# Performance work log

Hardware: AMD Instinct MI355X
Metric: run time of the kernel (lower is better)

Reference implementation:

```python
import jax, jax.numpy as jnp
import numpy as np

B, NIN, H1, H2, NOUT, COND, FC = 64, 512, 1024, 1024, 512, 64, 1


def _made_masks():
    rng = np.random.RandomState(0)
    d_in = np.arange(1, NIN + 1)
    d1 = rng.randint(1, NIN, size=H1)
    d2 = rng.randint(1, NIN, size=H2)
    d_out = np.arange(1, NOUT + 1)
    m0 = (d1[:, None] >= d_in[None, :]).astype(np.float32)   # (H1, NIN)
    m1 = (d2[:, None] >= d1[None, :]).astype(np.float32)     # (H2, H1)
    m2 = (d_out[:, None] > d2[None, :]).astype(np.float32)   # (NOUT, H2)
    return m0, m1, m2


def setup_inputs() -> dict:
    key = jax.random.key(0)
    ks = jax.random.split(key, 20)
    m0, m1, m2 = _made_masks()

    def lin(k, o, i):  # fan-in scaled weight
        return jax.random.normal(k, (o, i), jnp.float32) / np.float32(np.sqrt(i))

    def vec(k, n):
        return jax.random.normal(k, (n,), jnp.float32) * 0.01

    return {
        "x": jax.random.normal(ks[0], (B, NIN), jnp.float32),
        "u": jax.random.normal(ks[1], (B, COND), jnp.float32),
        "mask0": jnp.asarray(m0), "mask1": jnp.asarray(m1), "mask2": jnp.asarray(m2),
        "W0": lin(ks[2], H1, NIN), "W1": lin(ks[3], H2, H1), "W2": lin(ks[4], NOUT, H2),
        "a0_w": lin(ks[5], FC * NIN, COND), "a0_b": vec(ks[6], FC * NIN),
        "b0_w": lin(ks[7], FC * H1, COND), "b0_b": vec(ks[8], FC * H1),
        "a1_w": lin(ks[9], FC * H1, COND), "a1_b": vec(ks[10], FC * H1),
        "b1_w": lin(ks[11], FC * H2, COND), "b1_b": vec(ks[12], FC * H2),
        "a2_w": lin(ks[13], FC * H2, COND), "a2_b": vec(ks[14], FC * H2),
        "b2_w": lin(ks[15], FC * NOUT, COND), "b2_b": vec(ks[16], FC * NOUT),
    }


def _cml(x, u, W, m, aw, ab, bw, bb):
    # ConditionedMaskedLinear.forward
    Bb = x.shape[0]
    o, i = W.shape
    f1 = (u @ aw.T + ab).reshape(Bb, FC, i)      # (B, F, in)
    f2 = (u @ bw.T + bb).reshape(Bb, o, FC)      # (B, out, F)
    cond_mask = jax.nn.sigmoid(jnp.einsum('bfi,bof->boi', f1, f2)) * (m * W)
    return jnp.einsum('boi,bi->bo', cond_mask, x)


def reference(x, u, mask0, mask1, mask2, W0, W1, W2,
              a0_w, a0_b, b0_w, b0_b,
              a1_w, a1_b, b1_w, b1_b,
              a2_w, a2_b, b2_w, b2_b):
    # ConditionalStrNN.forward applies ONLY the ConditionedMaskedLinear layers
    # (activations/norms in net_list are skipped by the isinstance check).
    h = _cml(x, u, W0, mask0, a0_w, a0_b, b0_w, b0_b)
    h = _cml(h, u, W1, mask1, a1_w, a1_b, b1_w, b1_b)
    h = _cml(h, u, W2, mask2, a2_w, a2_b, b2_w, b2_b)
    return h
```

## Files before the change

### kernel.cpp

```cpp
#include <hip/hip_runtime.h>

#define BB    64
#define NIN   512
#define H1D   1024
#define H2D   1024
#define NOUTD 512
#define CONDD 64
#define L2E   1.4426950408889634f

__global__ __launch_bounds__(256) void prep_kernel(
    const float* __restrict__ x,  const float* __restrict__ u,
    const float* __restrict__ a0w, const float* __restrict__ a0b,
    const float* __restrict__ b0w, const float* __restrict__ b0b,
    const float* __restrict__ a1w, const float* __restrict__ a1b,
    const float* __restrict__ b1w, const float* __restrict__ b1b,
    const float* __restrict__ a2w, const float* __restrict__ a2b,
    const float* __restrict__ b2w, const float* __restrict__ b2b,
    float* __restrict__ AX0, float* __restrict__ AX1, float* __restrict__ AX2,
    float* __restrict__ C0t, float* __restrict__ C1t, float* __restrict__ C2t)
{
    __shared__ float lds[64 * 65];
    const int tid = threadIdx.x;
    const int bid = blockIdx.x;

    if (bid < 320) {
        for (int e = tid; e < BB * CONDD; e += 256)
            lds[(e & 63) * 65 + (e >> 6)] = u[e];
        __syncthreads();

        const int b   = tid & 63;
        const int wid = __builtin_amdgcn_readfirstlane(tid >> 6);
        const int r0  = bid * 16 + wid * 4;

        const float* w; const float* bias; float* out; int stride; float scale; int lr0;
        if      (r0 <  512) { w = a0w; bias = a0b; out = AX0; stride = 2; scale = L2E; lr0 = r0;        }
        else if (r0 < 1536) { w = b0w; bias = b0b; out = C0t; stride = 1; scale = 1.f; lr0 = r0 -  512; }
        else if (r0 < 2560) { w = a1w; bias = a1b; out = AX1; stride = 2; scale = L2E; lr0 = r0 - 1536; }
        else if (r0 < 3584) { w = b1w; bias = b1b; out = C1t; stride = 1; scale = 1.f; lr0 = r0 - 2560; }
        else if (r0 < 4608) { w = a2w; bias = a2b; out = AX2; stride = 2; scale = L2E; lr0 = r0 - 3584; }
        else                { w = b2w; bias = b2b; out = C2t; stride = 1; scale = 1.f; lr0 = r0 - 4608; }

        const float* __restrict__ w0 = w + (lr0 + 0) * CONDD;
        const float* __restrict__ w1 = w + (lr0 + 1) * CONDD;
        const float* __restrict__ w2 = w + (lr0 + 2) * CONDD;
        const float* __restrict__ w3 = w + (lr0 + 3) * CONDD;
        float acc0 = bias[lr0 + 0], acc1 = bias[lr0 + 1];
        float acc2 = bias[lr0 + 2], acc3 = bias[lr0 + 3];
        #pragma unroll
        for (int k = 0; k < CONDD; ++k) {
            const float uv = lds[k * 65 + b];
            acc0 = fmaf(w0[k], uv, acc0);
            acc1 = fmaf(w1[k], uv, acc1);
            acc2 = fmaf(w2[k], uv, acc2);
            acc3 = fmaf(w3[k], uv, acc3);
        }
        out[((lr0 + 0) * 64 + b) * stride] = acc0 * scale;
        out[((lr0 + 1) * 64 + b) * stride] = acc1 * scale;
        out[((lr0 + 2) * 64 + b) * stride] = acc2 * scale;
        out[((lr0 + 3) * 64 + b) * stride] = acc3 * scale;
    } else {
        const int i0 = (bid - 320) * 64;
        for (int e = tid; e < 64 * 64; e += 256) {
            int r = e >> 6, c = e & 63;
            lds[c * 65 + r] = x[r * NIN + i0 + c];
        }
        __syncthreads();
        for (int e = tid; e < 64 * 64; e += 256) {
            int r = e >> 6, c = e & 63;
            AX0[((i0 + r) * 64 + c) * 2 + 1] = lds[r * 65 + c];
        }
    }
}

template<int I, int OT, bool FINAL>
__device__ __forceinline__ void gated_body(
    const float2* __restrict__ AX, const float* __restrict__ Ct,
    const float*  __restrict__ M,  const float* __restrict__ W,
    float* __restrict__ out)
{
    constexpr int ICW = I / 8;
    const int tid = threadIdx.x;
    const int b   = tid & 63;
    const int wid = __builtin_amdgcn_readfirstlane(tid >> 6);
    const int o0  = blockIdx.x * OT;
    const int ibase = wid * ICW;

    float cc[OT], acc[OT];
    const float* __restrict__ mrow[OT];
    const float* __restrict__ wrow[OT];
    #pragma unroll
    for (int oo = 0; oo < OT; ++oo) {
        cc[oo]   = Ct[(o0 + oo) * 64 + b];
        mrow[oo] = M + (size_t)(o0 + oo) * I + ibase;
        wrow[oo] = W + (size_t)(o0 + oo) * I + ibase;
        acc[oo]  = 0.f;
    }
    const float2* __restrict__ axp = AX + (size_t)ibase * 64 + b;

    #pragma unroll 8
    for (int ii = 0; ii < ICW; ++ii) {
        const float2 ax = axp[(size_t)ii * 64];
        #pragma unroll
        for (int oo = 0; oo < OT; ++oo) {
            const float mw = mrow[oo][ii] * wrow[oo][ii];
            const float t  = __builtin_amdgcn_exp2f(-(ax.x * cc[oo]));
            const float s  = __builtin_amdgcn_rcpf(1.f + t);
            acc[oo] = fmaf(s, mw * ax.y, acc[oo]);
        }
    }

    __shared__ float red[8][OT][64];
    #pragma unroll
    for (int oo = 0; oo < OT; ++oo) red[wid][oo][b] = acc[oo];
    __syncthreads();
    if (tid < OT * 64) {
        const int oo = tid >> 6, bb = tid & 63;
        float v = 0.f;
        #pragma unroll
        for (int w8 = 0; w8 < 8; ++w8) v += red[w8][oo][bb];
        if (FINAL) out[bb * NOUTD + (o0 + oo)] = v;
        else       out[((o0 + oo) * 64 + bb) * 2 + 1] = v;
    }
}

__global__ __launch_bounds__(512) void gated_l1(
    const float2* __restrict__ AX, const float* __restrict__ Ct,
    const float* __restrict__ M, const float* __restrict__ W, float* __restrict__ out)
{ gated_body<NIN, 4, false>(AX, Ct, M, W, out); }

__global__ __launch_bounds__(512) void gated_l2(
    const float2* __restrict__ AX, const float* __restrict__ Ct,
    const float* __restrict__ M, const float* __restrict__ W, float* __restrict__ out)
{ gated_body<H1D, 4, false>(AX, Ct, M, W, out); }

__global__ __launch_bounds__(512) void gated_l3(
    const float2* __restrict__ AX, const float* __restrict__ Ct,
    const float* __restrict__ M, const float* __restrict__ W, float* __restrict__ out)
{ gated_body<H2D, 2, true>(AX, Ct, M, W, out); }

extern "C" void kernel_launch(void* const* d_in, const int* in_sizes, int n_in,
                              void* d_out, int out_size, void* d_ws, size_t ws_size,
                              hipStream_t stream) {
    (void)in_sizes; (void)n_in; (void)out_size; (void)ws_size;
    const float* x   = (const float*)d_in[0];
    const float* u   = (const float*)d_in[1];
    const float* m0  = (const float*)d_in[2];
    const float* m1  = (const float*)d_in[3];
    const float* m2  = (const float*)d_in[4];
    const float* W0  = (const float*)d_in[5];
    const float* W1  = (const float*)d_in[6];
    const float* W2  = (const float*)d_in[7];
    const float* a0w = (const float*)d_in[8];  const float* a0b = (const float*)d_in[9];
    const float* b0w = (const float*)d_in[10]; const float* b0b = (const float*)d_in[11];
    const float* a1w = (const float*)d_in[12]; const float* a1b = (const float*)d_in[13];
    const float* b1w = (const float*)d_in[14]; const float* b1b = (const float*)d_in[15];
    const float* a2w = (const float*)d_in[16]; const float* a2b = (const float*)d_in[17];
    const float* b2w = (const float*)d_in[18]; const float* b2b = (const float*)d_in[19];

    float* ws  = (float*)d_ws;
    float* AX0 = ws;
    float* AX1 = ws + 65536;
    float* AX2 = ws + 196608;
    float* C0t = ws + 327680;
    float* C1t = ws + 393216;
    float* C2t = ws + 458752;
    float* out = (float*)d_out;

    prep_kernel<<<328, 256, 0, stream>>>(x, u,
        a0w, a0b, b0w, b0b, a1w, a1b, b1w, b1b, a2w, a2b, b2w, b2b,
        AX0, AX1, AX2, C0t, C1t, C2t);

    gated_l1<<<H1D / 4,   512, 0, stream>>>((const float2*)AX0, C0t, m0, W0, AX1);
    gated_l2<<<H2D / 4,   512, 0, stream>>>((const float2*)AX1, C1t, m1, W1, AX2);
    gated_l3<<<NOUTD / 2, 512, 0, stream>>>((const float2*)AX2, C2t, m2, W2, out);
}
```

Before: 152.3 us.

## Fuse prep and three gated layers into one cooperative kernel with grid syncs

Replaces the four separate launches (prep plus three gated layers) with a single cooperative kernel of 256 blocks, using grid.sync between phases. The aim is to remove per-launch overhead and inter-kernel gaps. The x transpose is redone per warp with strided loads. Separately, the mask multiply becomes a bit-select on the weight, which assumes the mask values are 0 or 1. The grid-wide barriers add their own sync cost, and the launch_bounds(512,1) hint changes the register budget.

```diff
diff --git a/kernel.cpp b/kernel.cpp
--- a/kernel.cpp
+++ b/kernel.cpp
@@ -1,4 +1,7 @@
 #include <hip/hip_runtime.h>
+#include <hip/hip_cooperative_groups.h>
+
+namespace cg = cooperative_groups;
 
 #define BB    64
 #define NIN   512
@@ -8,81 +11,23 @@
 #define CONDD 64
 #define L2E   1.4426950408889634f
 
-__global__ __launch_bounds__(256) void prep_kernel(
-    const float* __restrict__ x,  const float* __restrict__ u,
-    const float* __restrict__ a0w, const float* __restrict__ a0b,
-    const float* __restrict__ b0w, const float* __restrict__ b0b,
-    const float* __restrict__ a1w, const float* __restrict__ a1b,
-    const float* __restrict__ b1w, const float* __restrict__ b1b,
-    const float* __restrict__ a2w, const float* __restrict__ a2b,
-    const float* __restrict__ b2w, const float* __restrict__ b2b,
-    float* __restrict__ AX0, float* __restrict__ AX1, float* __restrict__ AX2,
-    float* __restrict__ C0t, float* __restrict__ C1t, float* __restrict__ C2t)
-{
-    __shared__ float lds[64 * 65];
-    const int tid = threadIdx.x;
-    const int bid = blockIdx.x;
-
-    if (bid < 320) {
-        for (int e = tid; e < BB * CONDD; e += 256)
-            lds[(e & 63) * 65 + (e >> 6)] = u[e];
-        __syncthreads();
-
-        const int b   = tid & 63;
-        const int wid = __builtin_amdgcn_readfirstlane(tid >> 6);
-        const int r0  = bid * 16 + wid * 4;
-
-        const float* w; const float* bias; float* out; int stride; float scale; int lr0;
-        if      (r0 <  512) { w = a0w; bias = a0b; out = AX0; stride = 2; scale = L2E; lr0 = r0;        }
-        else if (r0 < 1536) { w = b0w; bias = b0b; out = C0t; stride = 1; scale = 1.f; lr0 = r0 -  512; }
-        else if (r0 < 2560) { w = a1w; bias = a1b; out = AX1; stride = 2; scale = L2E; lr0 = r0 - 1536; }
-        else if (r0 < 3584) { w = b1w; bias = b1b; out = C1t; stride = 1; scale = 1.f; lr0 = r0 - 2560; }
-        else if (r0 < 4608) { w = a2w; bias = a2b; out = AX2; stride = 2; scale = L2E; lr0 = r0 - 3584; }
-        else                { w = b2w; bias = b2b; out = C2t; stride = 1; scale = 1.f; lr0 = r0 - 4608; }
-
-        const float* __restrict__ w0 = w + (lr0 + 0) * CONDD;
-        const float* __restrict__ w1 = w + (lr0 + 1) * CONDD;
-        const float* __restrict__ w2 = w + (lr0 + 2) * CONDD;
-        const float* __restrict__ w3 = w + (lr0 + 3) * CONDD;
-        float acc0 = bias[lr0 + 0], acc1 = bias[lr0 + 1];
-        float acc2 = bias[lr0 + 2], acc3 = bias[lr0 + 3];
-        #pragma unroll
-        for (int k = 0; k < CONDD; ++k) {
-            const float uv = lds[k * 65 + b];
-            acc0 = fmaf(w0[k], uv, acc0);
-            acc1 = fmaf(w1[k], uv, acc1);
-            acc2 = fmaf(w2[k], uv, acc2);
-            acc3 = fmaf(w3[k], uv, acc3);
-        }
-        out[((lr0 + 0) * 64 + b) * stride] = acc0 * scale;
-        out[((lr0 + 1) * 64 + b) * stride] = acc1 * scale;
-        out[((lr0 + 2) * 64 + b) * stride] = acc2 * scale;
-        out[((lr0 + 3) * 64 + b) * stride] = acc3 * scale;
-    } else {
-        const int i0 = (bid - 320) * 64;
-        for (int e = tid; e < 64 * 64; e += 256) {
-            int r = e >> 6, c = e & 63;
-            lds[c * 65 + r] = x[r * NIN + i0 + c];
-        }
-        __syncthreads();
-        for (int e = tid; e < 64 * 64; e += 256) {
-            int r = e >> 6, c = e & 63;
-            AX0[((i0 + r) * 64 + c) * 2 + 1] = lds[r * 65 + c];
-        }
-    }
-}
+struct Params {
+    const float *x, *u, *m0, *m1, *m2, *W0, *W1, *W2;
+    const float *a0w, *a0b, *b0w, *b0b;
+    const float *a1w, *a1b, *b1w, *b1b;
+    const float *a2w, *a2b, *b2w, *b2b;
+    float *AX0, *AX1, *AX2, *C0t, *C1t, *C2t, *out;
+};
 
 template<int I, int OT, bool FINAL>
-__device__ __forceinline__ void gated_body(
+__device__ __forceinline__ void gated_phase(
     const float2* __restrict__ AX, const float* __restrict__ Ct,
     const float*  __restrict__ M,  const float* __restrict__ W,
-    float* __restrict__ out)
+    float* __restrict__ out, float (*red)[4][64],
+    int b, int wid, int tid)
 {
     constexpr int ICW = I / 8;
-    const int tid = threadIdx.x;
-    const int b   = tid & 63;
-    const int wid = __builtin_amdgcn_readfirstlane(tid >> 6);
-    const int o0  = blockIdx.x * OT;
+    const int o0    = blockIdx.x * OT;
     const int ibase = wid * ICW;
 
     float cc[OT], acc[OT];
@@ -102,14 +47,15 @@
         const float2 ax = axp[(size_t)ii * 64];
         #pragma unroll
         for (int oo = 0; oo < OT; ++oo) {
-            const float mw = mrow[oo][ii] * wrow[oo][ii];
+            const unsigned mb = __float_as_uint(mrow[oo][ii]);
+            const unsigned wb = __float_as_uint(wrow[oo][ii]);
+            const float mw = __uint_as_float(mb ? wb : 0u);
             const float t  = __builtin_amdgcn_exp2f(-(ax.x * cc[oo]));
             const float s  = __builtin_amdgcn_rcpf(1.f + t);
             acc[oo] = fmaf(s, mw * ax.y, acc[oo]);
         }
     }
 
-    __shared__ float red[8][OT][64];
     #pragma unroll
     for (int oo = 0; oo < OT; ++oo) red[wid][oo][b] = acc[oo];
     __syncthreads();
@@ -123,54 +69,99 @@
     }
 }
 
-__global__ __launch_bounds__(512) void gated_l1(
-    const float2* __restrict__ AX, const float* __restrict__ Ct,
-    const float* __restrict__ M, const float* __restrict__ W, float* __restrict__ out)
-{ gated_body<NIN, 4, false>(AX, Ct, M, W, out); }
+__global__ __launch_bounds__(512, 1) void fused_kernel(Params p)
+{
+    cg::grid_group grid = cg::this_grid();
+    __shared__ float uT[64 * 65];
+    __shared__ float red[8][4][64];
 
-__global__ __launch_bounds__(512) void gated_l2(
-    const float2* __restrict__ AX, const float* __restrict__ Ct,
-    const float* __restrict__ M, const float* __restrict__ W, float* __restrict__ out)
-{ gated_body<H1D, 4, false>(AX, Ct, M, W, out); }
+    const int tid = threadIdx.x;
+    const int b   = tid & 63;
+    const int wid = __builtin_amdgcn_readfirstlane(tid >> 6);
 
-__global__ __launch_bounds__(512) void gated_l3(
-    const float2* __restrict__ AX, const float* __restrict__ Ct,
-    const float* __restrict__ M, const float* __restrict__ W, float* __restrict__ out)
-{ gated_body<H2D, 2, true>(AX, Ct, M, W, out); }
+    for (int e = tid; e < BB * CONDD; e += 512)
+        uT[(e & 63) * 65 + (e >> 6)] = p.u[e];
+    __syncthreads();
+
+    const int gw = blockIdx.x * 8 + wid;
+    if (gw < 1280) {
+        const int r0 = gw * 4;
+        const float* w; const float* bias; float* outp; int stride; float scale; int lr0;
+        if      (r0 <  512) { w = p.a0w; bias = p.a0b; outp = p.AX0; stride = 2; scale = L2E; lr0 = r0;        }
+        else if (r0 < 1536) { w = p.b0w; bias = p.b0b; outp = p.C0t; stride = 1; scale = 1.f; lr0 = r0 -  512; }
+        else if (r0 < 2560) { w = p.a1w; bias = p.a1b; outp = p.AX1; stride = 2; scale = L2E; lr0 = r0 - 1536; }
+        else if (r0 < 3584) { w = p.b1w; bias = p.b1b; outp = p.C1t; stride = 1; scale = 1.f; lr0 = r0 - 2560; }
+        else if (r0 < 4608) { w = p.a2w; bias = p.a2b; outp = p.AX2; stride = 2; scale = L2E; lr0 = r0 - 3584; }
+        else                { w = p.b2w; bias = p.b2b; outp = p.C2t; stride = 1; scale = 1.f; lr0 = r0 - 4608; }
+
+        const float* __restrict__ w0 = w + (lr0 + 0) * CONDD;
+        const float* __restrict__ w1 = w + (lr0 + 1) * CONDD;
+        const float* __restrict__ w2 = w + (lr0 + 2) * CONDD;
+        const float* __restrict__ w3 = w + (lr0 + 3) * CONDD;
+        float acc0 = bias[lr0 + 0], acc1 = bias[lr0 + 1];
+        float acc2 = bias[lr0 + 2], acc3 = bias[lr0 + 3];
+        #pragma unroll
+        for (int k = 0; k < CONDD; ++k) {
+            const float uv = uT[k * 65 + b];
+            acc0 = fmaf(w0[k], uv, acc0);
+            acc1 = fmaf(w1[k], uv, acc1);
+            acc2 = fmaf(w2[k], uv, acc2);
+            acc3 = fmaf(w3[k], uv, acc3);
+        }
+        outp[((lr0 + 0) * 64 + b) * stride] = acc0 * scale;
+        outp[((lr0 + 1) * 64 + b) * stride] = acc1 * scale;
+        outp[((lr0 + 2) * 64 + b) * stride] = acc2 * scale;
+        outp[((lr0 + 3) * 64 + b) * stride] = acc3 * scale;
+    } else if (gw < 1344) {
+        const int i0 = (gw - 1280) * 8;
+        #pragma unroll
+        for (int r = 0; r < 8; ++r)
+            p.AX0[((i0 + r) * 64 + b) * 2 + 1] = p.x[b * NIN + i0 + r];
+    }
+    grid.sync();
+
+    gated_phase<NIN, 4, false>((const float2*)p.AX0, p.C0t, p.m0, p.W0,
+                               p.AX1, red, b, wid, tid);
+    grid.sync();
+
+    gated_phase<H1D, 4, false>((const float2*)p.AX1, p.C1t, p.m1, p.W1,
+                               p.AX2, red, b, wid, tid);
+    grid.sync();
+
+    gated_phase<H2D, 2, true>((const float2*)p.AX2, p.C2t, p.m2, p.W2,
+                              p.out, red, b, wid, tid);
+}
 
 extern "C" void kernel_launch(void* const* d_in, const int* in_sizes, int n_in,
                               void* d_out, int out_size, void* d_ws, size_t ws_size,
                               hipStream_t stream) {
     (void)in_sizes; (void)n_in; (void)out_size; (void)ws_size;
-    const float* x   = (const float*)d_in[0];
-    const float* u   = (const float*)d_in[1];
-    const float* m0  = (const float*)d_in[2];
-    const float* m1  = (const float*)d_in[3];
-    const float* m2  = (const float*)d_in[4];
-    const float* W0  = (const float*)d_in[5];
-    const float* W1  = (const float*)d_in[6];
-    const float* W2  = (const float*)d_in[7];
-    const float* a0w = (const float*)d_in[8];  const float* a0b = (const float*)d_in[9];
-    const float* b0w = (const float*)d_in[10]; const float* b0b = (const float*)d_in[11];
-    const float* a1w = (const float*)d_in[12]; const float* a1b = (const float*)d_in[13];
-    const float* b1w = (const float*)d_in[14]; const float* b1b = (const float*)d_in[15];
-    const float* a2w = (const float*)d_in[16]; const float* a2b = (const float*)d_in[17];
-    const float* b2w = (const float*)d_in[18]; const float* b2b = (const float*)d_in[19];
 
-    float* ws  = (float*)d_ws;
-    float* AX0 = ws;
-    float* AX1 = ws + 65536;
-    float* AX2 = ws + 196608;
-    float* C0t = ws + 327680;
-    float* C1t = ws + 393216;
-    float* C2t = ws + 458752;
-    float* out = (float*)d_out;
+    float* ws = (float*)d_ws;
+    Params p;
+    p.x   = (const float*)d_in[0];
+    p.u   = (const float*)d_in[1];
+    p.m0  = (const float*)d_in[2];
+    p.m1  = (const float*)d_in[3];
+    p.m2  = (const float*)d_in[4];
+    p.W0  = (const float*)d_in[5];
+    p.W1  = (const float*)d_in[6];
+    p.W2  = (const float*)d_in[7];
+    p.a0w = (const float*)d_in[8];  p.a0b = (const float*)d_in[9];
+    p.b0w = (const float*)d_in[10]; p.b0b = (const float*)d_in[11];
+    p.a1w = (const float*)d_in[12]; p.a1b = (const float*)d_in[13];
+    p.b1w = (const float*)d_in[14]; p.b1b = (const float*)d_in[15];
+    p.a2w = (const float*)d_in[16]; p.a2b = (const float*)d_in[17];
+    p.b2w = (const float*)d_in[18]; p.b2b = (const float*)d_in[19];
+    p.AX0 = ws;
+    p.AX1 = ws + 65536;
+    p.AX2 = ws + 196608;
+    p.C0t = ws + 327680;
+    p.C1t = ws + 393216;
+    p.C2t = ws + 458752;
+    p.out = (float*)d_out;
 
-    prep_kernel<<<328, 256, 0, stream>>>(x, u,
-        a0w, a0b, b0w, b0b, a1w, a1b, b1w, b1b, a2w, a2b, b2w, b2b,
-        AX0, AX1, AX2, C0t, C1t, C2t);
-
-    gated_l1<<<H1D / 4,   512, 0, stream>>>((const float2*)AX0, C0t, m0, W0, AX1);
-    gated_l2<<<H2D / 4,   512, 0, stream>>>((const float2*)AX1, C1t, m1, W1, AX2);
-    gated_l3<<<NOUTD / 2, 512, 0, stream>>>((const float2*)AX2, C2t, m2, W2, out);
+    void* kargs[] = { (void*)&p };
+    hipLaunchCooperativeKernel((void*)fused_kernel, dim3(256), dim3(512),
+                               kargs, 0, stream);
 }
```

Measured after the change: 280.1 us. 83.9% more time.
